# Kernel optimization log

Measured on AMD Instinct MI355X. Metric: run time of the kernel, lower is better.

The kernel has to match this reference:

```python
import jax, jax.numpy as jnp
import numpy as np

EPS = 1e-8  # matches F.cosine_similarity eps clamp

def _cosine_gram(x):
    # row-normalize with eps clamp, then Gram matrix == pairwise cosine similarity
    norms = jnp.maximum(jnp.linalg.norm(x, axis=-1, keepdims=True), EPS)
    xn = x / norms
    return xn @ xn.T  # [N, N]

def setup_inputs() -> dict:
    key = jax.random.key(0)
    k1, k2 = jax.random.split(key)
    N, D = 4096, 512
    return {
        "cosine_distance_latent": jax.random.normal(k1, (N, D), dtype=jnp.float32),
        "mse_latent": jax.random.normal(k2, (N, D), dtype=jnp.float32),
    }

def reference(cosine_distance_latent, mse_latent):
    # cosine distance matrices: (sim - 1) * -1 == 1 - sim
    cd = 1.0 - _cosine_gram(cosine_distance_latent)  # target
    ed = 1.0 - _cosine_gram(mse_latent)              # predicted
    # KL(softmax(cd) || softmax(ed)) per row, then mean
    log_t = jax.nn.log_softmax(cd, axis=-1)
    log_p = jax.nn.log_softmax(ed, axis=-1)
    t = jnp.exp(log_t)
    kl = jnp.sum(t * (log_t - log_p), axis=-1)
    return jnp.mean(kl)
```

## Files before the change

kernel.cpp:

```cpp
#include <hip/hip_runtime.h>
#include <math.h>

#define NROWS 4096
#define DIM   512
#define UNIT  128
#define NP    (NROWS / UNIT)
#define NTILES (NP * (NP + 1) / 2)
#define KSTEPS (DIM / 32)
#define NSLOT NP

typedef __bf16 bf16x8 __attribute__((ext_vector_type(8)));
typedef float  f32x4  __attribute__((ext_vector_type(4)));

#define GL16(G, L) __builtin_amdgcn_global_load_lds( \
    (const __attribute__((address_space(1))) void*)(G), \
    (__attribute__((address_space(3))) void*)(L), 16, 0, 0)

__global__ __launch_bounds__(256)
void normalize_kernel(const float* __restrict__ X, const float* __restrict__ Y,
                      __bf16* __restrict__ Xn, __bf16* __restrict__ Yn)
{
    const int wid  = threadIdx.x >> 6;
    const int lane = threadIdx.x & 63;
    const int row  = blockIdx.x * 4 + wid;
    const float* src = blockIdx.y ? Y : X;
    __bf16*      dst = blockIdx.y ? Yn : Xn;

    const float4* s4 = reinterpret_cast<const float4*>(src + (size_t)row * DIM);
    float4 v0 = s4[lane * 2 + 0];
    float4 v1 = s4[lane * 2 + 1];
    float ss = v0.x*v0.x + v0.y*v0.y + v0.z*v0.z + v0.w*v0.w
             + v1.x*v1.x + v1.y*v1.y + v1.z*v1.z + v1.w*v1.w;
    #pragma unroll
    for (int m = 1; m < 64; m <<= 1) ss += __shfl_xor(ss, m);
    const float scale = 1.0f / fmaxf(sqrtf(ss), 1e-8f);

    bf16x8 o;
    o[0] = (__bf16)(v0.x * scale); o[1] = (__bf16)(v0.y * scale);
    o[2] = (__bf16)(v0.z * scale); o[3] = (__bf16)(v0.w * scale);
    o[4] = (__bf16)(v1.x * scale); o[5] = (__bf16)(v1.y * scale);
    o[6] = (__bf16)(v1.z * scale); o[7] = (__bf16)(v1.w * scale);
    *reinterpret_cast<bf16x8*>(dst + (size_t)row * DIM + lane * 8) = o;
}

__global__ __launch_bounds__(256, 2)
void gram_kl_kernel(const __bf16* __restrict__ Xn, const __bf16* __restrict__ Yn,
                    float4* __restrict__ partials)
{
    __shared__ char lds[65536];

    const int tid  = threadIdx.x;
    const int wid  = tid >> 6;
    const int lane = tid & 63;
    const int m  = wid >> 1;
    const int iq = wid & 1;

    const int glin = (blockIdx.x & 7) * (NTILES / 8) + (blockIdx.x >> 3);
    int p = (int)((sqrtf((float)(8 * glin + 1)) - 1.0f) * 0.5f);
    while ((p + 1) * (p + 2) / 2 <= glin) ++p;
    while (p * (p + 1) / 2 > glin) --p;
    const int q = glin - p * (p + 1) / 2;
    const int i0 = p * UNIT;
    const int j0 = q * UNIT;

    const int xnib = (((tid & 3) ^ ((tid >> 3) & 3)) << 4);
    const int r0 = tid >> 2;
    const size_t so_i = ((size_t)(i0 + r0) << 10) + xnib;
    const size_t so_j = ((size_t)(j0 + r0) << 10) + xnib;
    const int wbase = wid * 1024;

    const char* bx = (const char*)Xn;
    const char* by = (const char*)Yn;

    auto STAGE = [&](int st, int ks) {
        char* base = &lds[st * 32768];
        const size_t ko = (size_t)ks << 6;
        const size_t h = (size_t)64 << 10;
        GL16(bx + so_j + ko,     base + 0 * 8192 + wbase);
        GL16(bx + so_j + h + ko, base + 0 * 8192 + 4096 + wbase);
        GL16(by + so_j + ko,     base + 1 * 8192 + wbase);
        GL16(by + so_j + h + ko, base + 1 * 8192 + 4096 + wbase);
        GL16(bx + so_i + ko,     base + 2 * 8192 + wbase);
        GL16(bx + so_i + h + ko, base + 2 * 8192 + 4096 + wbase);
        GL16(by + so_i + ko,     base + 3 * 8192 + wbase);
        GL16(by + so_i + h + ko, base + 3 * 8192 + 4096 + wbase);
    };

    const int rdx = ((lane & 15) << 6) + ((((lane >> 4) ^ ((lane >> 1) & 3))) << 4);
    const int jbase = m * 8192;
    const int ibase = 16384 + m * 8192 + iq * 4096;

    f32x4 acc[8][4];
    #pragma unroll
    for (int fj = 0; fj < 8; ++fj)
        #pragma unroll
        for (int fi = 0; fi < 4; ++fi)
            acc[fj][fi] = f32x4{0.f, 0.f, 0.f, 0.f};

    STAGE(0, 0);

    for (int s = 0; s < KSTEPS; ++s) {
        asm volatile("s_waitcnt vmcnt(0)" ::: "memory");
        __builtin_amdgcn_s_barrier();
        asm volatile("" ::: "memory");

        const char* base = &lds[(s & 1) * 32768];
        bf16x8 aJ[8], bI[4];
        #pragma unroll
        for (int fj = 0; fj < 8; ++fj)
            aJ[fj] = *reinterpret_cast<const bf16x8*>(base + jbase + fj * 1024 + rdx);
        #pragma unroll
        for (int fi = 0; fi < 4; ++fi)
            bI[fi] = *reinterpret_cast<const bf16x8*>(base + ibase + fi * 1024 + rdx);

        if (s + 1 < KSTEPS) STAGE((s + 1) & 1, s + 1);

        #pragma unroll
        for (int fj = 0; fj < 8; ++fj)
            #pragma unroll
            for (int fi = 0; fi < 4; ++fi)
                acc[fj][fi] = __builtin_amdgcn_mfma_f32_16x16x32_bf16(aJ[fj], bI[fi], acc[fj][fi], 0, 0, 0);
    }

    char*  chunk = &lds[0];
    float* jpart = reinterpret_cast<float*>(&lds[8192]);

    const int sub = lane >> 4;
    float Si[4] = {0,0,0,0}, Ui[4] = {0,0,0,0}, Vi[4] = {0,0,0,0}, Qi[4] = {0,0,0,0};

    __syncthreads();

    #pragma unroll
    for (int fj = 0; fj < 8; ++fj) {
        if (m == 1) {
            #pragma unroll
            for (int fi = 0; fi < 4; ++fi)
                *reinterpret_cast<f32x4*>(chunk + iq * 4096 + fi * 1024 + lane * 16) = acc[fj][fi];
        }
        __syncthreads();
        if (m == 0) {
            float js[4][4];
            #pragma unroll
            for (int r = 0; r < 4; ++r) { js[r][0]=0; js[r][1]=0; js[r][2]=0; js[r][3]=0; }
            #pragma unroll
            for (int fi = 0; fi < 4; ++fi) {
                const f32x4 pb = *reinterpret_cast<const f32x4*>(chunk + iq * 4096 + fi * 1024 + lane * 16);
                #pragma unroll
                for (int r = 0; r < 4; ++r) {
                    const float a = -acc[fj][fi][r];
                    const float b = -pb[r];
                    const float ea = __expf(a);
                    const float eb = __expf(b);
                    Si[fi] += ea; Ui[fi] += ea * a; Vi[fi] += ea * b; Qi[fi] += eb;
                    js[r][0] += ea; js[r][1] += ea * a; js[r][2] += ea * b; js[r][3] += eb;
                }
            }
            if (p != q) {
                #pragma unroll
                for (int r = 0; r < 4; ++r)
                    #pragma unroll
                    for (int c = 0; c < 4; ++c) {
                        #pragma unroll
                        for (int mk = 1; mk <= 8; mk <<= 1)
                            js[r][c] += __shfl_xor(js[r][c], mk);
                    }
                if ((lane & 15) == 0) {
                    #pragma unroll
                    for (int r = 0; r < 4; ++r) {
                        const int j = fj * 16 + sub * 4 + r;
                        #pragma unroll
                        for (int c = 0; c < 4; ++c)
                            jpart[(iq * 128 + j) * 4 + c] = js[r][c];
                    }
                }
            }
        }
        __syncthreads();
    }

    if (m == 0) {
        #pragma unroll
        for (int fi = 0; fi < 4; ++fi) {
            #pragma unroll
            for (int mk = 16; mk <= 32; mk <<= 1) {
                Si[fi] += __shfl_xor(Si[fi], mk);
                Ui[fi] += __shfl_xor(Ui[fi], mk);
                Vi[fi] += __shfl_xor(Vi[fi], mk);
                Qi[fi] += __shfl_xor(Qi[fi], mk);
            }
        }
        if (lane < 16) {
            #pragma unroll
            for (int fi = 0; fi < 4; ++fi) {
                const int row = i0 + iq * 64 + fi * 16 + lane;
                partials[(size_t)row * NSLOT + q] = float4{Si[fi], Ui[fi], Vi[fi], Qi[fi]};
            }
        }
    }
    __syncthreads();

    if (p != q && wid == 0) {
        #pragma unroll
        for (int h = 0; h < 2; ++h) {
            const int j = h * 64 + lane;
            float4 v;
            v.x = jpart[(0 * 128 + j) * 4 + 0] + jpart[(1 * 128 + j) * 4 + 0];
            v.y = jpart[(0 * 128 + j) * 4 + 1] + jpart[(1 * 128 + j) * 4 + 1];
            v.z = jpart[(0 * 128 + j) * 4 + 2] + jpart[(1 * 128 + j) * 4 + 2];
            v.w = jpart[(0 * 128 + j) * 4 + 3] + jpart[(1 * 128 + j) * 4 + 3];
            partials[(size_t)(j0 + j) * NSLOT + p] = v;
        }
    }
}

__global__ __launch_bounds__(256)
void merge_kernel(const float4* __restrict__ partials, float* __restrict__ blocksum)
{
    __shared__ float w[4];
    const int row = blockIdx.x * 256 + threadIdx.x;
    float S = 0.f, U = 0.f, V = 0.f, Q = 0.f;
    #pragma unroll
    for (int s = 0; s < NSLOT; ++s) {
        const float4 pp = partials[(size_t)row * NSLOT + s];
        S += pp.x; U += pp.y; V += pp.z; Q += pp.w;
    }
    float kl = (U - V) / S - logf(S) + logf(Q);
    #pragma unroll
    for (int mm = 1; mm < 64; mm <<= 1) kl += __shfl_xor(kl, mm);
    if ((threadIdx.x & 63) == 0) w[threadIdx.x >> 6] = kl;
    __syncthreads();
    if (threadIdx.x == 0) blocksum[blockIdx.x] = w[0] + w[1] + w[2] + w[3];
}

__global__ __launch_bounds__(64)
void reduce_kernel(const float* __restrict__ blocksum, float* __restrict__ out)
{
    float v = (threadIdx.x < 16) ? blocksum[threadIdx.x] : 0.f;
    #pragma unroll
    for (int mm = 1; mm < 16; mm <<= 1) v += __shfl_xor(v, mm);
    if (threadIdx.x == 0) out[0] = v / (float)NROWS;
}

extern "C" void kernel_launch(void* const* d_in, const int* in_sizes, int n_in,
                              void* d_out, int out_size, void* d_ws, size_t ws_size,
                              hipStream_t stream)
{
    const float* X = (const float*)d_in[0];
    const float* Y = (const float*)d_in[1];
    float* out = (float*)d_out;

    char* ws = (char*)d_ws;
    const size_t mat_bytes = (size_t)NROWS * DIM * sizeof(__bf16);
    __bf16* Xn = (__bf16*)ws;
    __bf16* Yn = (__bf16*)(ws + mat_bytes);
    float4* partials = (float4*)(ws + 2 * mat_bytes);
    float* blocksum = (float*)(ws + 2 * mat_bytes + (size_t)NROWS * NSLOT * sizeof(float4));

    normalize_kernel<<<dim3(NROWS / 4, 2), 256, 0, stream>>>(X, Y, Xn, Yn);
    gram_kl_kernel<<<NTILES, 256, 0, stream>>>(Xn, Yn, partials);
    merge_kernel<<<NROWS / 256, 256, 0, stream>>>(partials, blocksum);
    reduce_kernel<<<1, 64, 0, stream>>>(blocksum, out);
}
```

Measured before the change: 70.90 us.

## Split gram tiles into 128x64 grains for finer load balance and occupancy

Replaces the 128x128 triangular tile decomposition with 128x64 grains (1056 blocks), cutting per-block LDS to 48KB and raising launch bounds to 3 blocks per CU. The partial-slot indexing and merge loop are rewritten for the new grain layout, with each row reading a row-dependent number of slots. The aim is to fill the GPU better and cut tail imbalance from the 528 large tiles. In exchange, the symmetric trick now saves less, since diagonal grains redo half their work, and each block loads the i-rows again for half as much output.

```diff
diff --git a/kernel.cpp b/kernel.cpp
--- a/kernel.cpp
+++ b/kernel.cpp
@@ -3,11 +3,12 @@
 
 #define NROWS 4096
 #define DIM   512
-#define UNIT  128
-#define NP    (NROWS / UNIT)
-#define NTILES (NP * (NP + 1) / 2)
+#define UNIT_I 128
+#define UNIT_J 64
+#define NPI   (NROWS / UNIT_I)
+#define NGRAINS 1056
 #define KSTEPS (DIM / 32)
-#define NSLOT NP
+#define NSLOT 64
 
 typedef __bf16 bf16x8 __attribute__((ext_vector_type(8)));
 typedef float  f32x4  __attribute__((ext_vector_type(4)));
@@ -43,11 +44,11 @@
     *reinterpret_cast<bf16x8*>(dst + (size_t)row * DIM + lane * 8) = o;
 }
 
-__global__ __launch_bounds__(256, 2)
+__global__ __launch_bounds__(256, 3)
 void gram_kl_kernel(const __bf16* __restrict__ Xn, const __bf16* __restrict__ Yn,
                     float4* __restrict__ partials)
 {
-    __shared__ char lds[65536];
+    __shared__ char lds[49152];
 
     const int tid  = threadIdx.x;
     const int wid  = tid >> 6;
@@ -55,13 +56,14 @@
     const int m  = wid >> 1;
     const int iq = wid & 1;
 
-    const int glin = (blockIdx.x & 7) * (NTILES / 8) + (blockIdx.x >> 3);
-    int p = (int)((sqrtf((float)(8 * glin + 1)) - 1.0f) * 0.5f);
-    while ((p + 1) * (p + 2) / 2 <= glin) ++p;
-    while (p * (p + 1) / 2 > glin) --p;
-    const int q = glin - p * (p + 1) / 2;
-    const int i0 = p * UNIT;
-    const int j0 = q * UNIT;
+    const int gl = (blockIdx.x & 7) * (NGRAINS / 8) + (blockIdx.x >> 3);
+    int p = (int)((sqrtf((float)(4 * gl + 1)) - 1.0f) * 0.5f);
+    while ((p + 1) * (p + 2) <= gl) ++p;
+    while (p * (p + 1) > gl) --p;
+    const int q = gl - p * (p + 1);
+    const int i0 = p * UNIT_I;
+    const int j0 = q * UNIT_J;
+    const int diag = (p == (q >> 1));
 
     const int xnib = (((tid & 3) ^ ((tid >> 3) & 3)) << 4);
     const int r0 = tid >> 2;
@@ -73,26 +75,22 @@
     const char* by = (const char*)Yn;
 
     auto STAGE = [&](int st, int ks) {
-        char* base = &lds[st * 32768];
+        char* base = &lds[st * 24576];
         const size_t ko = (size_t)ks << 6;
         const size_t h = (size_t)64 << 10;
-        GL16(bx + so_j + ko,     base + 0 * 8192 + wbase);
-        GL16(bx + so_j + h + ko, base + 0 * 8192 + 4096 + wbase);
-        GL16(by + so_j + ko,     base + 1 * 8192 + wbase);
-        GL16(by + so_j + h + ko, base + 1 * 8192 + 4096 + wbase);
-        GL16(bx + so_i + ko,     base + 2 * 8192 + wbase);
-        GL16(bx + so_i + h + ko, base + 2 * 8192 + 4096 + wbase);
-        GL16(by + so_i + ko,     base + 3 * 8192 + wbase);
-        GL16(by + so_i + h + ko, base + 3 * 8192 + 4096 + wbase);
+        GL16(bx + so_j + ko,     base + 0     + wbase);
+        GL16(by + so_j + ko,     base + 4096  + wbase);
+        GL16(bx + so_i + ko,     base + 8192  + wbase);
+        GL16(bx + so_i + h + ko, base + 12288 + wbase);
+        GL16(by + so_i + ko,     base + 16384 + wbase);
+        GL16(by + so_i + h + ko, base + 20480 + wbase);
     };
 
     const int rdx = ((lane & 15) << 6) + ((((lane >> 4) ^ ((lane >> 1) & 3))) << 4);
-    const int jbase = m * 8192;
-    const int ibase = 16384 + m * 8192 + iq * 4096;
-
-    f32x4 acc[8][4];
-    #pragma unroll
-    for (int fj = 0; fj < 8; ++fj)
+
+    f32x4 acc[4][4];
+    #pragma unroll
+    for (int fj = 0; fj < 4; ++fj)
         #pragma unroll
         for (int fi = 0; fi < 4; ++fi)
             acc[fj][fi] = f32x4{0.f, 0.f, 0.f, 0.f};
@@ -104,19 +102,22 @@
         __builtin_amdgcn_s_barrier();
         asm volatile("" ::: "memory");
 
-        const char* base = &lds[(s & 1) * 32768];
-        bf16x8 aJ[8], bI[4];
-        #pragma unroll
-        for (int fj = 0; fj < 8; ++fj)
-            aJ[fj] = *reinterpret_cast<const bf16x8*>(base + jbase + fj * 1024 + rdx);
+        const char* base = &lds[(s & 1) * 24576];
+        const char* jb = base + m * 4096;
+        const char* ib = base + 8192 + m * 8192 + iq * 4096;
+
+        bf16x8 aJ[4], bI[4];
+        #pragma unroll
+        for (int fj = 0; fj < 4; ++fj)
+            aJ[fj] = *reinterpret_cast<const bf16x8*>(jb + fj * 1024 + rdx);
         #pragma unroll
         for (int fi = 0; fi < 4; ++fi)
-            bI[fi] = *reinterpret_cast<const bf16x8*>(base + ibase + fi * 1024 + rdx);
+            bI[fi] = *reinterpret_cast<const bf16x8*>(ib + fi * 1024 + rdx);
 
         if (s + 1 < KSTEPS) STAGE((s + 1) & 1, s + 1);
 
         #pragma unroll
-        for (int fj = 0; fj < 8; ++fj)
+        for (int fj = 0; fj < 4; ++fj)
             #pragma unroll
             for (int fi = 0; fi < 4; ++fi)
                 acc[fj][fi] = __builtin_amdgcn_mfma_f32_16x16x32_bf16(aJ[fj], bI[fi], acc[fj][fi], 0, 0, 0);
@@ -131,7 +132,7 @@
     __syncthreads();
 
     #pragma unroll
-    for (int fj = 0; fj < 8; ++fj) {
+    for (int fj = 0; fj < 4; ++fj) {
         if (m == 1) {
             #pragma unroll
             for (int fi = 0; fi < 4; ++fi)
@@ -155,7 +156,7 @@
                     js[r][0] += ea; js[r][1] += ea * a; js[r][2] += ea * b; js[r][3] += eb;
                 }
             }
-            if (p != q) {
+            if (!diag) {
                 #pragma unroll
                 for (int r = 0; r < 4; ++r)
                     #pragma unroll
@@ -170,7 +171,7 @@
                         const int j = fj * 16 + sub * 4 + r;
                         #pragma unroll
                         for (int c = 0; c < 4; ++c)
-                            jpart[(iq * 128 + j) * 4 + c] = js[r][c];
+                            jpart[(iq * 64 + j) * 4 + c] = js[r][c];
                     }
                 }
             }
@@ -199,17 +200,15 @@
     }
     __syncthreads();
 
-    if (p != q && wid == 0) {
-        #pragma unroll
-        for (int h = 0; h < 2; ++h) {
-            const int j = h * 64 + lane;
-            float4 v;
-            v.x = jpart[(0 * 128 + j) * 4 + 0] + jpart[(1 * 128 + j) * 4 + 0];
-            v.y = jpart[(0 * 128 + j) * 4 + 1] + jpart[(1 * 128 + j) * 4 + 1];
-            v.z = jpart[(0 * 128 + j) * 4 + 2] + jpart[(1 * 128 + j) * 4 + 2];
-            v.w = jpart[(0 * 128 + j) * 4 + 3] + jpart[(1 * 128 + j) * 4 + 3];
-            partials[(size_t)(j0 + j) * NSLOT + p] = v;
-        }
+    if (!diag && wid == 0) {
+        const int j = lane;
+        const int mslot = (q >> 1) + p + 1;
+        float4 v;
+        v.x = jpart[(0 * 64 + j) * 4 + 0] + jpart[(1 * 64 + j) * 4 + 0];
+        v.y = jpart[(0 * 64 + j) * 4 + 1] + jpart[(1 * 64 + j) * 4 + 1];
+        v.z = jpart[(0 * 64 + j) * 4 + 2] + jpart[(1 * 64 + j) * 4 + 2];
+        v.w = jpart[(0 * 64 + j) * 4 + 3] + jpart[(1 * 64 + j) * 4 + 3];
+        partials[(size_t)(j0 + j) * NSLOT + mslot] = v;
     }
 }
 
@@ -218,9 +217,9 @@
 {
     __shared__ float w[4];
     const int row = blockIdx.x * 256 + threadIdx.x;
+    const int nsl = (row >> 7) + 33;
     float S = 0.f, U = 0.f, V = 0.f, Q = 0.f;
-    #pragma unroll
-    for (int s = 0; s < NSLOT; ++s) {
+    for (int s = 0; s < nsl; ++s) {
         const float4 pp = partials[(size_t)row * NSLOT + s];
         S += pp.x; U += pp.y; V += pp.z; Q += pp.w;
     }
@@ -257,7 +256,7 @@
     float* blocksum = (float*)(ws + 2 * mat_bytes + (size_t)NROWS * NSLOT * sizeof(float4));
 
     normalize_kernel<<<dim3(NROWS / 4, 2), 256, 0, stream>>>(X, Y, Xn, Yn);
-    gram_kl_kernel<<<NTILES, 256, 0, stream>>>(Xn, Yn, partials);
+    gram_kl_kernel<<<NGRAINS, 256, 0, stream>>>(Xn, Yn, partials);
     merge_kernel<<<NROWS / 256, 256, 0, stream>>>(partials, blocksum);
     reduce_kernel<<<1, 64, 0, stream>>>(blocksum, out);
 }
```

New measurement: 67.44 us. 1.05x faster.
